# Kernel optimization log

Measured on AMD Instinct MI355X. Metric: run time of the kernel, lower is better.

The kernel has to match this reference:

```python
import jax, jax.numpy as jnp
import numpy as np

B, N, H, W = 128, 16384, 512, 512  # frames, points/frame, image height/width


def setup_inputs() -> dict:
    key = jax.random.key(0)
    k1, k2 = jax.random.split(key)
    pts = jax.random.uniform(k1, (B, N, 3), dtype=jnp.float32)
    # columns: x in [0, W-1], y in [0, H-1], intensity in [0, 1]
    outputs = jnp.concatenate(
        [pts[..., 0:1] * (W - 1), pts[..., 1:2] * (H - 1), pts[..., 2:3]], axis=-1
    )
    targets = jax.random.uniform(k2, (B, H, W), dtype=jnp.float32)
    return {"outputs": outputs, "targets": targets}


def _rasterize(outputs, h, w):
    """Bilinear splat of (x, y, intensity) points into a [B, h, w] image."""
    b, n, _ = outputs.shape
    x = jnp.clip(outputs[..., 0], 0.0, w - 1)
    y = jnp.clip(outputs[..., 1], 0.0, h - 1)
    inten = outputs[..., 2]
    x0f = jnp.floor(x)
    y0f = jnp.floor(y)
    fx = x - x0f  # fractional offsets -> bilinear weights
    fy = y - y0f
    x0 = x0f.astype(jnp.int32)
    y0 = y0f.astype(jnp.int32)
    x1 = jnp.minimum(x0 + 1, w - 1)
    y1 = jnp.minimum(y0 + 1, h - 1)
    bidx = jnp.broadcast_to(jnp.arange(b, dtype=jnp.int32)[:, None], (b, n))
    img = jnp.zeros((b, h, w), dtype=outputs.dtype)
    img = img.at[bidx, y0, x0].add(inten * (1 - fx) * (1 - fy))
    img = img.at[bidx, y0, x1].add(inten * fx * (1 - fy))
    img = img.at[bidx, y1, x0].add(inten * (1 - fx) * fy)
    img = img.at[bidx, y1, x1].add(inten * fx * fy)
    return img


def reference(outputs, targets):
    h, w = targets.shape[1], targets.shape[2]
    output_image = _rasterize(outputs, h, w)
    return jnp.mean((output_image - targets) ** 2)
```

## Files before the change

kernel.cpp:

```cpp
#include <hip/hip_runtime.h>

constexpr int B = 128;
constexpr int N = 16384;
constexpr int H = 512;
constexpr int W = 512;
constexpr int HW = H * W;
constexpr long long TOT = (long long)B * HW;

constexpr int TROWS = 8;
constexpr int NTILES = H / TROWS;
constexpr int NBUCKETS = B * NTILES;
constexpr int CAP = 512;
constexpr int NGROUPS = B * N / 4;
constexpr int BIN_BLOCKS = NGROUPS / 512;
constexpr int TPB = 4;
constexpr int PTS_BLOCKS = NBUCKETS / TPB;

__global__ void __launch_bounds__(512) k_zero(unsigned int* __restrict__ cnt) {
    cnt[blockIdx.x * 512 + threadIdx.x] = 0u;
}

__global__ void __launch_bounds__(512) k_bin(const float4* __restrict__ pts,
                                             float4* __restrict__ buckets,
                                             unsigned int* __restrict__ cnt) {
    __shared__ unsigned int lcnt[NTILES];
    __shared__ unsigned int lbase[NTILES];

    int tid = blockIdx.x * 512 + threadIdx.x;
    int frame = tid >> 12;
    int fb = frame * NTILES;

    if (threadIdx.x < NTILES) lcnt[threadIdx.x] = 0;
    __syncthreads();

    float4 a = pts[tid * 3 + 0];
    float4 b = pts[tid * 3 + 1];
    float4 c = pts[tid * 3 + 2];

    float xs[4] = {a.x, a.w, b.z, c.y};
    float ys[4] = {a.y, b.x, b.w, c.z};
    float is[4] = {a.z, b.y, c.x, c.w};

    int tb0[4], sl0[4], tb1[4], sl1[4];
#pragma unroll
    for (int k = 0; k < 4; ++k) {
        float x = fminf(fmaxf(xs[k], 0.0f), (float)(W - 1));
        float y = fminf(fmaxf(ys[k], 0.0f), (float)(H - 1));
        xs[k] = x; ys[k] = y;
        int y0 = (int)floorf(y);
        int y1 = min(y0 + 1, H - 1);
        int t0 = y0 >> 3;
        int t1 = y1 >> 3;
        tb0[k] = t0;
        sl0[k] = (int)atomicAdd(&lcnt[t0], 1u);
        if (t1 != t0) {
            tb1[k] = t1;
            sl1[k] = (int)atomicAdd(&lcnt[t1], 1u);
        } else {
            tb1[k] = -1; sl1[k] = 0;
        }
    }
    __syncthreads();

    if (threadIdx.x < NTILES)
        lbase[threadIdx.x] = atomicAdd(&cnt[fb + threadIdx.x], lcnt[threadIdx.x]);
    __syncthreads();

#pragma unroll
    for (int k = 0; k < 4; ++k) {
        float4 rec = make_float4(xs[k], ys[k], is[k], 0.0f);
        unsigned s0 = lbase[tb0[k]] + (unsigned)sl0[k];
        if (s0 < (unsigned)CAP)
            buckets[(size_t)(fb + tb0[k]) * CAP + s0] = rec;
        if (tb1[k] >= 0) {
            unsigned s1 = lbase[tb1[k]] + (unsigned)sl1[k];
            if (s1 < (unsigned)CAP)
                buckets[(size_t)(fb + tb1[k]) * CAP + s1] = rec;
        }
    }
}

__global__ void __launch_bounds__(256) k_pts(const float4* __restrict__ buckets,
                                             const unsigned int* __restrict__ cnt,
                                             const float* __restrict__ tgt,
                                             double* __restrict__ ppts) {
    __shared__ float tile[TROWS * W];
    __shared__ int ncache[TPB];
    __shared__ double sacc[4];

    int tid = threadIdx.x;
    int base = blockIdx.x * TPB;
    int frame = base >> 6;
    const float* tf = tgt + (size_t)frame * HW;

    if (tid < TPB) ncache[tid] = (int)min(cnt[base + tid], (unsigned)CAP);

    float4* t4 = (float4*)tile;
    float4 z = make_float4(0.f, 0.f, 0.f, 0.f);
#pragma unroll
    for (int k = 0; k < TROWS * W / 4 / 256; ++k)
        t4[tid + k * 256] = z;
    __syncthreads();

    double acc = 0.0;
#pragma unroll
    for (int j = 0; j < TPB; ++j) {
        int bid = base + j;
        int r0 = (bid & (NTILES - 1)) * TROWS;
        int n = ncache[j];
        const float4* bp = buckets + (size_t)bid * CAP;

        const float4* tg4 = (const float4*)(tf + (size_t)r0 * W);
        float4 ta = tg4[tid];
        float4 tb = tg4[tid + 256];
        float4 tc = tg4[tid + 512];
        float4 td = tg4[tid + 768];

        bool v0 = tid < n, v1 = tid + 256 < n;
        float4 p0 = v0 ? bp[tid]       : make_float4(0.f, 0.f, 0.f, 0.f);
        float4 p1 = v1 ? bp[tid + 256] : make_float4(0.f, 0.f, 0.f, 0.f);

        float q0 = ta.x * ta.x + ta.y * ta.y + ta.z * ta.z + ta.w * ta.w;
        float q1 = tb.x * tb.x + tb.y * tb.y + tb.z * tb.z + tb.w * tb.w;
        float q2 = tc.x * tc.x + tc.y * tc.y + tc.z * tc.z + tc.w * tc.w;
        float q3 = td.x * td.x + td.y * td.y + td.z * td.z + td.w * td.w;

        float facc = 0.0f;
#pragma unroll
        for (int s = 0; s < 2; ++s) {
            bool valid = s == 0 ? v0 : v1;
            if (!valid) continue;
            float4 p = s == 0 ? p0 : p1;
            float x = p.x, y = p.y, inten = p.z;
            float x0f = floorf(x), y0f = floorf(y);
            float fx = x - x0f, fy = y - y0f;
            int x0 = (int)x0f, y0 = (int)y0f;
            int x1 = min(x0 + 1, W - 1);
            int y1 = min(y0 + 1, H - 1);
            int ra = y0 - r0, rb = y1 - r0;
            float w00 = inten * (1.0f - fx) * (1.0f - fy);
            float w01 = inten * fx * (1.0f - fy);
            float w10 = inten * (1.0f - fx) * fy;
            float w11 = inten * fx * fy;
            if ((unsigned)ra < (unsigned)TROWS) {
                float t00 = tf[y0 * W + x0];
                float t01 = tf[y0 * W + x1];
                float o0 = atomicAdd(&tile[ra * W + x0], w00);
                float o1 = atomicAdd(&tile[ra * W + x1], w01);
                facc += w00 * (w00 + 2.0f * o0) - 2.0f * w00 * t00;
                facc += w01 * (w01 + 2.0f * o1) - 2.0f * w01 * t01;
            }
            if ((unsigned)rb < (unsigned)TROWS) {
                float t10 = tf[y1 * W + x0];
                float t11 = tf[y1 * W + x1];
                float o2 = atomicAdd(&tile[rb * W + x0], w10);
                float o3 = atomicAdd(&tile[rb * W + x1], w11);
                facc += w10 * (w10 + 2.0f * o2) - 2.0f * w10 * t10;
                facc += w11 * (w11 + 2.0f * o3) - 2.0f * w11 * t11;
            }
        }
        acc += (double)facc + (double)(q0 + q1) + (double)(q2 + q3);
        __syncthreads();

#pragma unroll
        for (int s = 0; s < 2; ++s) {
            bool valid = s == 0 ? v0 : v1;
            if (!valid) continue;
            float4 p = s == 0 ? p0 : p1;
            float x = p.x, y = p.y;
            int x0 = (int)floorf(x), y0 = (int)floorf(y);
            int x1 = min(x0 + 1, W - 1);
            int y1 = min(y0 + 1, H - 1);
            int ra = y0 - r0, rb = y1 - r0;
            if ((unsigned)ra < (unsigned)TROWS) {
                tile[ra * W + x0] = 0.0f;
                tile[ra * W + x1] = 0.0f;
            }
            if ((unsigned)rb < (unsigned)TROWS) {
                tile[rb * W + x0] = 0.0f;
                tile[rb * W + x1] = 0.0f;
            }
        }
        __syncthreads();
    }

    for (int off = 32; off > 0; off >>= 1)
        acc += __shfl_down(acc, off, 64);
    int lane = tid & 63;
    int wave = tid >> 6;
    if (lane == 0) sacc[wave] = acc;
    __syncthreads();
    if (tid == 0)
        ppts[blockIdx.x] = sacc[0] + sacc[1] + sacc[2] + sacc[3];
}

__global__ void __launch_bounds__(512) k_final(const double* __restrict__ ppts,
                                               float* __restrict__ out) {
    double acc = 0.0;
    for (int i = threadIdx.x; i < PTS_BLOCKS; i += 512)
        acc += ppts[i];
    for (int off = 32; off > 0; off >>= 1)
        acc += __shfl_down(acc, off, 64);
    __shared__ double sacc[8];
    int lane = threadIdx.x & 63;
    int wave = threadIdx.x >> 6;
    if (lane == 0) sacc[wave] = acc;
    __syncthreads();
    if (threadIdx.x == 0) {
        double s = 0.0;
#pragma unroll
        for (int wv = 0; wv < 8; ++wv) s += sacc[wv];
        out[0] = (float)(s / (double)TOT);
    }
}

extern "C" void kernel_launch(void* const* d_in, const int* in_sizes, int n_in,
                              void* d_out, int out_size, void* d_ws, size_t ws_size,
                              hipStream_t stream) {
    const float* pts = (const float*)d_in[0];
    const float* tgt = (const float*)d_in[1];
    float* out = (float*)d_out;

    unsigned int* cnt = (unsigned int*)d_ws;
    double* ppts = (double*)((char*)d_ws + 32768);
    float4* buckets = (float4*)((char*)d_ws + 65536);

    k_zero<<<NBUCKETS / 512, 512, 0, stream>>>(cnt);
    k_bin<<<BIN_BLOCKS, 512, 0, stream>>>((const float4*)pts, buckets, cnt);
    k_pts<<<PTS_BLOCKS, 256, 0, stream>>>(buckets, cnt, tgt, ppts);
    k_final<<<1, 512, 0, stream>>>(ppts, out);
}
```

Measured before the change: 87.05 us.

## Split target sum-of-squares into a separate streaming reduction kernel

Measured after the change: 98.09 us. 12.7% more time.

```diff
diff --git a/kernel.cpp b/kernel.cpp
--- a/kernel.cpp
+++ b/kernel.cpp
@@ -15,6 +15,7 @@
 constexpr int BIN_BLOCKS = NGROUPS / 512;
 constexpr int TPB = 4;
 constexpr int PTS_BLOCKS = NBUCKETS / TPB;
+constexpr int SQ_BLOCKS = 4096;
 
 __global__ void __launch_bounds__(512) k_zero(unsigned int* __restrict__ cnt) {
     cnt[blockIdx.x * 512 + threadIdx.x] = 0u;
@@ -80,6 +81,40 @@
     }
 }
 
+__global__ void __launch_bounds__(256) k_sq(const float4* __restrict__ tgt4,
+                                            double* __restrict__ psq) {
+    int tid = threadIdx.x;
+    size_t base = (size_t)blockIdx.x * 2048 + tid;
+
+    float4 v[8];
+#pragma unroll
+    for (int k = 0; k < 8; ++k)
+        v[k] = tgt4[base + (size_t)k * 256];
+
+    float a0 = 0.f, a1 = 0.f, a2 = 0.f, a3 = 0.f;
+#pragma unroll
+    for (int k = 0; k < 8; k += 4) {
+        a0 += v[k + 0].x * v[k + 0].x + v[k + 0].y * v[k + 0].y +
+              v[k + 0].z * v[k + 0].z + v[k + 0].w * v[k + 0].w;
+        a1 += v[k + 1].x * v[k + 1].x + v[k + 1].y * v[k + 1].y +
+              v[k + 1].z * v[k + 1].z + v[k + 1].w * v[k + 1].w;
+        a2 += v[k + 2].x * v[k + 2].x + v[k + 2].y * v[k + 2].y +
+              v[k + 2].z * v[k + 2].z + v[k + 2].w * v[k + 2].w;
+        a3 += v[k + 3].x * v[k + 3].x + v[k + 3].y * v[k + 3].y +
+              v[k + 3].z * v[k + 3].z + v[k + 3].w * v[k + 3].w;
+    }
+    double acc = (double)((a0 + a1) + (a2 + a3));
+
+    for (int off = 32; off > 0; off >>= 1)
+        acc += __shfl_down(acc, off, 64);
+    __shared__ double sacc[4];
+    int lane = tid & 63, wave = tid >> 6;
+    if (lane == 0) sacc[wave] = acc;
+    __syncthreads();
+    if (tid == 0)
+        psq[blockIdx.x] = sacc[0] + sacc[1] + sacc[2] + sacc[3];
+}
+
 __global__ void __launch_bounds__(256) k_pts(const float4* __restrict__ buckets,
                                              const unsigned int* __restrict__ cnt,
                                              const float* __restrict__ tgt,
@@ -110,20 +145,9 @@
         int n = ncache[j];
         const float4* bp = buckets + (size_t)bid * CAP;
 
-        const float4* tg4 = (const float4*)(tf + (size_t)r0 * W);
-        float4 ta = tg4[tid];
-        float4 tb = tg4[tid + 256];
-        float4 tc = tg4[tid + 512];
-        float4 td = tg4[tid + 768];
-
         bool v0 = tid < n, v1 = tid + 256 < n;
         float4 p0 = v0 ? bp[tid]       : make_float4(0.f, 0.f, 0.f, 0.f);
         float4 p1 = v1 ? bp[tid + 256] : make_float4(0.f, 0.f, 0.f, 0.f);
-
-        float q0 = ta.x * ta.x + ta.y * ta.y + ta.z * ta.z + ta.w * ta.w;
-        float q1 = tb.x * tb.x + tb.y * tb.y + tb.z * tb.z + tb.w * tb.w;
-        float q2 = tc.x * tc.x + tc.y * tc.y + tc.z * tc.z + tc.w * tc.w;
-        float q3 = td.x * td.x + td.y * td.y + td.z * td.z + td.w * td.w;
 
         float facc = 0.0f;
 #pragma unroll
@@ -159,7 +183,7 @@
                 facc += w11 * (w11 + 2.0f * o3) - 2.0f * w11 * t11;
             }
         }
-        acc += (double)facc + (double)(q0 + q1) + (double)(q2 + q3);
+        acc += (double)facc;
         __syncthreads();
 
 #pragma unroll
@@ -194,9 +218,12 @@
         ppts[blockIdx.x] = sacc[0] + sacc[1] + sacc[2] + sacc[3];
 }
 
-__global__ void __launch_bounds__(512) k_final(const double* __restrict__ ppts,
+__global__ void __launch_bounds__(512) k_final(const double* __restrict__ psq,
+                                               const double* __restrict__ ppts,
                                                float* __restrict__ out) {
     double acc = 0.0;
+    for (int i = threadIdx.x; i < SQ_BLOCKS; i += 512)
+        acc += psq[i];
     for (int i = threadIdx.x; i < PTS_BLOCKS; i += 512)
         acc += ppts[i];
     for (int off = 32; off > 0; off >>= 1)
@@ -222,11 +249,13 @@
     float* out = (float*)d_out;
 
     unsigned int* cnt = (unsigned int*)d_ws;
-    double* ppts = (double*)((char*)d_ws + 32768);
-    float4* buckets = (float4*)((char*)d_ws + 65536);
+    double* psq  = (double*)((char*)d_ws + 32768);
+    double* ppts = (double*)((char*)d_ws + 65536);
+    float4* buckets = (float4*)((char*)d_ws + 131072);
 
     k_zero<<<NBUCKETS / 512, 512, 0, stream>>>(cnt);
     k_bin<<<BIN_BLOCKS, 512, 0, stream>>>((const float4*)pts, buckets, cnt);
+    k_sq<<<SQ_BLOCKS, 256, 0, stream>>>((const float4*)tgt, psq);
     k_pts<<<PTS_BLOCKS, 256, 0, stream>>>(buckets, cnt, tgt, ppts);
-    k_final<<<1, 512, 0, stream>>>(ppts, out);
-}
+    k_final<<<1, 512, 0, stream>>>(psq, ppts, out);
+}
```
